# Kernel tuning notes

Hardware: AMD Instinct MI355X
Metric: run time of the kernel (lower is better)

The kernel has to match this reference:

```python
import jax, jax.numpy as jnp
import numpy as np

CLS_NUM = 2
SF = 8.0
STRIDE = 5
NO_OBJ_SCALE = 1.0
GAMMA = 1.0
B, C, H, W = 16, 8, 256, 256
NT = 256


def setup_inputs() -> dict:
    key = jax.random.key(0)
    k1, k2, k3, k4, k5, k6, k7 = jax.random.split(key, 7)
    predict = jax.random.normal(k1, (B, C, H, W), dtype=jnp.float32)
    b = jax.random.randint(k2, (NT,), 0, B).astype(jnp.float32)
    c = jax.random.randint(k3, (NT,), 0, CLS_NUM).astype(jnp.float32)
    cx = jax.random.uniform(k4, (NT,)) * (W * SF)   # image-scale coords
    cy = jax.random.uniform(k5, (NT,)) * (H * SF)
    wh = jax.random.uniform(k6, (NT, 2)) * 72.0 + 8.0  # box sizes in [8,80] px
    ang = (jax.random.uniform(k7, (NT,)) - 0.5) * np.pi
    targets = jnp.stack([b, c, cx, cy, wh[:, 0], wh[:, 1], ang], axis=1).astype(jnp.float32)
    return {"predict": predict, "targets": targets}


def _forward_loss(predict, targets):
    nB, nC, nH, nW = predict.shape
    N = targets.shape[0]
    pred = jnp.transpose(predict, (0, 2, 3, 1))  # [B,H,W,C]
    half = (STRIDE - 1) / 2.0
    x = jax.nn.sigmoid(pred[..., 0]) * STRIDE - half
    y = jax.nn.sigmoid(pred[..., 1]) * STRIDE - half
    w_p = pred[..., 2]
    h_p = pred[..., 3]
    p = jax.nn.sigmoid(pred[..., 4]) * 2.0 - 1.0
    q = jax.nn.sigmoid(pred[..., 5]) * 2.0 - 1.0

    # targets are detached in the torch code (numpy) -> no grad path
    tg = jax.lax.stop_gradient(targets)
    b_idx = tg[:, 0].astype(jnp.int32)
    cls_t = tg[:, 1].astype(jnp.int32)
    cx = tg[:, 2] / SF
    cy = tg[:, 3] / SF
    bw = tg[:, 4] / SF
    bh = tg[:, 5] / SF
    ang = tg[:, 6]
    ca, sa = jnp.cos(ang), jnp.sin(ang)

    # --- rotated-box rasterization for all boxes at once: [N,H,W] ---
    gx = jnp.arange(nW, dtype=jnp.float32) + 0.5
    gy = jnp.arange(nH, dtype=jnp.float32) + 0.5
    vx = gx[None, None, :] * ca[:, None, None] + gy[None, :, None] * sa[:, None, None]
    vy = -gx[None, None, :] * sa[:, None, None] + gy[None, :, None] * ca[:, None, None]
    bx = cx * ca + cy * sa
    by = -cx * sa + cy * ca
    x3 = (bx - bh / 2)[:, None, None]
    x4 = (bx + bh / 2)[:, None, None]
    y3 = (by - bw / 2)[:, None, None]
    y4 = (by + bw / 2)[:, None, None]
    inbox = (vx >= x3) & (vx <= x4) & (vy >= y3) & (vy <= y4)
    inexp = (vx >= x3 - 0.5) & (vx <= x4 + 0.5) & (vy >= y3 - 0.5) & (vy <= y4 + 0.5)

    # --- candidate grid cells around each box center (stride+1 window) ---
    lower = 0.5 - STRIDE / 2.0  # -2.0
    upper = 0.5 + STRIDE / 2.0  # 3.0
    K = STRIDE + 1
    i0 = jnp.floor(cx + lower).astype(jnp.int32)
    j0 = jnp.floor(cy + lower).astype(jnp.int32)
    I = jnp.broadcast_to((i0[:, None] + jnp.arange(K))[:, None, :], (N, K, K))
    J = jnp.broadcast_to((j0[:, None] + jnp.arange(K))[:, :, None], (N, K, K))
    ox = cx[:, None, None] - I.astype(jnp.float32)
    oy = cy[:, None, None] - J.astype(jnp.float32)
    inb = (I >= 0) & (I < nW) & (J >= 0) & (J < nH)
    off = (ox >= lower) & (ox <= upper) & (oy >= lower) & (oy <= upper)
    Ic = jnp.clip(I, 0, nW - 1)
    Jc = jnp.clip(J, 0, nH - 1)
    lin = ((b_idx[:, None, None] * nH + Jc) * nW + Ic).reshape(-1)
    SIZE = nB * nH * nW
    oxf = ox.reshape(-1)
    oyf = oy.reshape(-1)
    logw_f = jnp.broadcast_to(jnp.log(bw)[:, None, None], (N, K, K)).reshape(-1)
    logh_f = jnp.broadcast_to(jnp.log(bh)[:, None, None], (N, K, K)).reshape(-1)
    ang_f = jnp.broadcast_to(ang[:, None, None], (N, K, K)).reshape(-1)
    vflat = jnp.minimum(jnp.abs(oxf - 0.5), jnp.abs(oyf - 0.5))  # assignment priority

    total = jnp.float32(0.0)
    for c_id in range(CLS_NUM):
        cm = cls_t == c_id
        heat = jax.ops.segment_sum((inbox & cm[:, None, None]).astype(jnp.float32), b_idx, num_segments=nB) > 0
        cold = jax.ops.segment_sum((inexp & cm[:, None, None]).astype(jnp.float32), b_idx, num_segments=nB) == 0
        validf = (inb & off & cm[:, None, None]).reshape(-1)
        heat_at = heat.reshape(-1)[lin]
        cold_at = cold.reshape(-1)[lin]
        # noobj cleared at window cells overlapping the expanded rotated boxes
        clear_idx = jnp.where(validf & ~cold_at, lin, SIZE)
        noobj = jnp.ones(SIZE + 1, jnp.float32).at[clear_idx].set(0.0)[:SIZE]
        # per-cell min-priority box assignment (scatter-min + winner gather)
        elig = validf & heat_at
        vbig = jnp.where(elig, vflat, jnp.inf)
        minv = jnp.full(SIZE, jnp.inf, jnp.float32).at[lin].min(vbig)
        win = elig & (vbig <= minv[lin])
        widx = jnp.where(win, lin, SIZE)

        def scat(vals):
            return jnp.zeros(SIZE + 1, jnp.float32).at[widx].set(vals)[:SIZE]

        obj = jnp.zeros(SIZE + 1, jnp.float32).at[widx].set(1.0)[:SIZE]
        tx = scat(oxf).reshape(nB, nH, nW)
        ty = scat(oyf).reshape(nB, nH, nW)
        tw = scat(logw_f).reshape(nB, nH, nW)
        th = scat(logh_f).reshape(nB, nH, nW)
        ta = scat(ang_f).reshape(nB, nH, nW)
        obj = obj.reshape(nB, nH, nW)
        noobj = (noobj.reshape(nB, nH, nW)) * (1.0 - obj)

        n_obj = jnp.sum(obj)
        dn = jnp.maximum(n_obj, 1.0)
        n_no = jnp.sum(noobj)
        dno = jnp.maximum(n_no, 1.0)
        z = pred[..., 6 + c_id]  # conf logit; BCE(sigmoid(z), t) == softplus(+/-z)
        loss_conf_obj = jnp.sum(obj * jax.nn.softplus(-z)) / dn
        loss_conf_noobj = jnp.sum(noobj * jax.nn.softplus(z)) / dno

        def om(t):
            return jnp.sum(obj * t) / dn

        loss_x = om((x - tx) ** 2)
        loss_y = om((y - ty) ** 2)
        loss_w = om((w_p - tw) ** 2)
        loss_h = om((h_p - th) ** 2)
        wt = th - tw  # log(h)-log(w) at obj cells
        awt = jnp.abs(wt) ** GAMMA
        loss_angle = om(awt * (jnp.abs(p - jnp.cos(2.0 * ta)) + jnp.abs(q - jnp.sin(2.0 * ta))))
        loss_ring = om(jnp.abs(wt) * jnp.abs(p * p + q * q - 1.0))
        cls_loss = (loss_conf_obj + NO_OBJ_SCALE * loss_conf_noobj
                    + loss_x + loss_y + loss_w + loss_h + loss_angle + loss_ring)
        total = total + jnp.where(n_obj > 0, cls_loss, 0.0)
    return total


def reference(predict, targets):
    return _forward_loss(predict, targets)
```

## Files before the change

### kernel.cpp

```cpp
#include <hip/hip_runtime.h>
#include <math.h>

#define NTGT 256
#define NB 16
#define NH 256
#define NW 256
#define GSIZE (NB * NH * NW)

#define NENTBLK 36
#define NCONFBLK 256
#define PART 0
#define ENT  256

__device__ __forceinline__ float softplusf(float z) {
    return fmaxf(z, 0.0f) + log1pf(expf(-fabsf(z)));
}
__device__ __forceinline__ float sigmoidf(float t) {
    return 1.0f / (1.0f + expf(-t));
}

__global__ __launch_bounds__(256) void fused_main(const float* __restrict__ predict,
                                                  const float* __restrict__ targets,
                                                  float* __restrict__ ws) {
#pragma clang fp contract(off)
    const int t = threadIdx.x;

    if (blockIdx.x >= NENTBLK) {
        __shared__ float red[4];
        const int cb = blockIdx.x - NENTBLK;
        const int j = cb * 256 + t;
        const int ch  = 6 + ((j >> 14) & 1);
        const int pos = j & 16383;
        const int bhi = j >> 15;
        float s = 0.0f;
        for (int it = 0; it < 8; ++it) {
            const int b = it * 2 + bhi;
            const float4 v = *reinterpret_cast<const float4*>(
                predict + (size_t)(b * 8 + ch) * 65536 + (size_t)pos * 4);
            s += softplusf(v.x) + softplusf(v.y) + softplusf(v.z) + softplusf(v.w);
        }
        for (int o = 32; o > 0; o >>= 1) s += __shfl_down(s, o, 64);
        if ((t & 63) == 0) red[t >> 6] = s;
        __syncthreads();
        if (t == 0) ws[PART + cb] = red[0] + red[1] + red[2] + red[3];
        return;
    }

    __shared__ float s_raw[NTGT * 7];
    __shared__ float s_cx[NTGT], s_cy[NTGT], s_ca[NTGT], s_sa[NTGT];
    __shared__ float s_x3[NTGT], s_x4[NTGT], s_y3[NTGT], s_y4[NTGT];
    __shared__ int   s_i0[NTGT], s_j0[NTGT], s_g[NTGT], s_gl[NTGT];
    __shared__ int   s_gs[33];
    __shared__ int   cntg[32];
    __shared__ float blksum[16];
    __shared__ unsigned blkcnt[4];

    for (int i = t; i < NTGT * 7; i += 256) s_raw[i] = targets[i];
    if (t < 32) cntg[t] = 0;
    if (t < 16) blksum[t] = 0.0f;
    if (t >= 16 && t < 20) blkcnt[t - 16] = 0u;
    __syncthreads();

    {
        const float* T = &s_raw[t * 7];
        const int b   = (int)T[0];
        const int cls = (int)T[1];
        const float cx = T[2] * 0.125f, cy = T[3] * 0.125f;
        const float bw = T[4] * 0.125f, bh = T[5] * 0.125f;
        float sa, ca;
        sincosf(T[6], &sa, &ca);
        const float bx =  cx * ca + cy * sa;
        const float by = -cx * sa + cy * ca;
        const int g = b * 2 + cls;
        s_cx[t] = cx;  s_cy[t] = cy;
        s_ca[t] = ca;  s_sa[t] = sa;
        s_x3[t] = bx - bh * 0.5f;  s_x4[t] = bx + bh * 0.5f;
        s_y3[t] = by - bw * 0.5f;  s_y4[t] = by + bw * 0.5f;
        s_i0[t] = (int)floorf(cx - 2.0f);
        s_j0[t] = (int)floorf(cy - 2.0f);
        s_g[t]  = g;
        const int pos = atomicAdd(&cntg[g], 1);
        __syncthreads();
        if (t == 0) {
            int s = 0;
            for (int i = 0; i < 32; ++i) { s_gs[i] = s; s += cntg[i]; }
            s_gs[32] = s;
        }
        __syncthreads();
        s_gl[s_gs[g] + pos] = t;
    }
    __syncthreads();

    const int e = blockIdx.x * 256 + t;
    const int n = e / 36;
    const int sub = e - n * 36;
    const int kj = sub / 6;
    const int ki = sub - kj * 6;

    const int g = s_g[n];
    const int cls = g & 1;
    const int b = g >> 1;
    const int I = s_i0[n] + ki, J = s_j0[n] + kj;
    const float cx = s_cx[n], cy = s_cy[n];
    const float ox = cx - (float)I;
    const float oy = cy - (float)J;

    const bool validf = (I >= 0 && I < NW && J >= 0 && J < NH) &&
                        (ox >= -2.0f && ox <= 3.0f && oy >= -2.0f && oy <= 3.0f);

    bool isOwner = false, isWinC = false;
    const int gs = s_gs[g], ge = s_gs[g + 1];
    if (validf) {
        const float vfl = fminf(fabsf(ox - 0.5f), fabsf(oy - 0.5f));
        const unsigned long long mypack =
            ((unsigned long long)__float_as_uint(vfl) << 32) | (unsigned)e;
        unsigned long long best = mypack;
        int ownmin = e;
        for (int p = gs; p < ge; ++p) {
            const int m = s_gl[p];
            if (m == n) continue;
            const int kip = I - s_i0[m];
            if (kip < 0 || kip > 5) continue;
            const int kjp = J - s_j0[m];
            if (kjp < 0 || kjp > 5) continue;
            const float oxp = s_cx[m] - (float)I;
            const float oyp = s_cy[m] - (float)J;
            if (!(oxp >= -2.0f && oxp <= 3.0f && oyp >= -2.0f && oyp <= 3.0f)) continue;
            const int ep = (m * 6 + kjp) * 6 + kip;
            ownmin = min(ownmin, ep);
            const float vflp = fminf(fabsf(oxp - 0.5f), fabsf(oyp - 0.5f));
            const unsigned long long pk =
                ((unsigned long long)__float_as_uint(vflp) << 32) | (unsigned)ep;
            if (pk < best) best = pk;
        }
        isOwner = (ownmin == e);
        isWinC  = (best == mypack);
    }

    bool heat = false, anyexp = false;
    if (isOwner || isWinC) {
        const float gx = (float)I + 0.5f;
        const float gy = (float)J + 0.5f;
        for (int p = gs; p < ge; ++p) {
            const int m = s_gl[p];
            const float ca = s_ca[m], sa = s_sa[m];
            const float vx =  gx * ca + gy * sa;
            const float vy = -gx * sa + gy * ca;
            const float x3 = s_x3[m], x4 = s_x4[m];
            const float y3 = s_y3[m], y4 = s_y4[m];
            heat   |= (vx >= x3 && vx <= x4 && vy >= y3 && vy <= y4);
            anyexp |= (vx >= x3 - 0.5f && vx <= x4 + 0.5f &&
                       vy >= y3 - 0.5f && vy <= y4 + 0.5f);
        }
    }

    const size_t base = (size_t)b * 8 * 65536 + (size_t)J * 256 + (size_t)I;
    const bool doClear = isOwner && anyexp;
    const bool doWin   = isWinC && heat;

    float spz = 0.0f;
    if (doClear) spz = softplusf(predict[base + (size_t)(6 + cls) * 65536]);
    float v0 = (doClear && cls == 0) ? spz : 0.0f;
    float v1 = (doClear && cls == 1) ? spz : 0.0f;
    for (int o = 32; o > 0; o >>= 1) {
        v0 += __shfl_down(v0, o, 64);
        v1 += __shfl_down(v1, o, 64);
    }
    const unsigned long long m0 = __ballot(doClear && cls == 0);
    const unsigned long long m1 = __ballot(doClear && cls == 1);
    if ((t & 63) == 0) {
        if (v0 != 0.0f) atomicAdd(&blksum[14], v0);
        if (v1 != 0.0f) atomicAdd(&blksum[15], v1);
        if (m0) atomicAdd(&blkcnt[2], (unsigned)__popcll(m0));
        if (m1) atomicAdd(&blkcnt[3], (unsigned)__popcll(m1));
    }

    if (doWin) {
        const float p0 = predict[base];
        const float p1 = predict[base + 65536];
        const float p2 = predict[base + 2 * 65536];
        const float p3 = predict[base + 3 * 65536];
        const float p4 = predict[base + 4 * 65536];
        const float p5 = predict[base + 5 * 65536];
        const float z  = predict[base + (size_t)(6 + cls) * 65536];
        const float bw = s_raw[n * 7 + 4] * 0.125f;
        const float bh = s_raw[n * 7 + 5] * 0.125f;
        const float ang = s_raw[n * 7 + 6];
        const float xs = sigmoidf(p0) * 5.0f - 2.0f;
        const float ys = sigmoidf(p1) * 5.0f - 2.0f;
        const float pp = sigmoidf(p4) * 2.0f - 1.0f;
        const float qq = sigmoidf(p5) * 2.0f - 1.0f;
        const float tw = logf(bw), th = logf(bh);
        const float wt = th - tw, awt = fabsf(wt);
        float s2a, c2a;
        sincosf(2.0f * ang, &s2a, &c2a);
        atomicAdd(&blksum[0 + cls],  softplusf(-z));
        atomicAdd(&blksum[2 + cls],  (xs - ox) * (xs - ox));
        atomicAdd(&blksum[4 + cls],  (ys - oy) * (ys - oy));
        atomicAdd(&blksum[6 + cls],  (p2 - tw) * (p2 - tw));
        atomicAdd(&blksum[8 + cls],  (p3 - th) * (p3 - th));
        atomicAdd(&blksum[10 + cls], awt * (fabsf(pp - c2a) + fabsf(qq - s2a)));
        atomicAdd(&blksum[12 + cls], awt * fabsf(pp * pp + qq * qq - 1.0f));
        atomicAdd(&blkcnt[cls], 1u);
    }

    __syncthreads();
    if (t < 16) {
        ws[ENT + blockIdx.x * 20 + t] = blksum[t];
    } else if (t < 20) {
        ws[ENT + blockIdx.x * 20 + t] = (float)blkcnt[t - 16];
    }
}

__global__ __launch_bounds__(256) void final_kernel(const float* __restrict__ ws,
                                                    float* __restrict__ out) {
    __shared__ float r0[256], r1[256];
    __shared__ float esum[20];
    const int t = threadIdx.x;
    if (t < 20) esum[t] = 0.0f;
    const float v = ws[PART + t];
    const int c = (t >> 6) & 1;
    r0[t] = c ? 0.0f : v;
    r1[t] = c ? v : 0.0f;
    __syncthreads();
    for (int idx = t; idx < NENTBLK * 20; idx += 256) {
        const int slot = idx % 20;
        atomicAdd(&esum[slot], ws[ENT + idx]);
    }
    for (int o = 128; o > 0; o >>= 1) {
        __syncthreads();
        if (t < o) { r0[t] += r0[t + o]; r1[t] += r1[t + o]; }
    }
    __syncthreads();
    if (t == 0) {
        const float sAll[2] = { r0[0], r1[0] };
        float total = 0.0f;
        for (int c2 = 0; c2 < 2; ++c2) {
            const float nobj = esum[16 + c2];
            if (nobj > 0.0f) {
                const float dn  = nobj;
                const float dno = fmaxf((float)GSIZE - esum[18 + c2], 1.0f);
                total += esum[0 + c2] / dn
                       + (sAll[c2] - esum[14 + c2]) / dno
                       + (esum[2 + c2] + esum[4 + c2] + esum[6 + c2]
                          + esum[8 + c2] + esum[10 + c2] + esum[12 + c2]) / dn;
            }
        }
        out[0] = total;
    }
}

extern "C" void kernel_launch(void* const* d_in, const int* in_sizes, int n_in,
                              void* d_out, int out_size, void* d_ws, size_t ws_size,
                              hipStream_t stream) {
    const float* predict = (const float*)d_in[0];
    const float* targets = (const float*)d_in[1];
    float* out = (float*)d_out;
    float* ws = (float*)d_ws;

    fused_main<<<NENTBLK + NCONFBLK, 256, 0, stream>>>(predict, targets, ws);
    final_kernel<<<1, 256, 0, stream>>>(ws, out);
}
```

Measured before the change: 19.44 us.

## Merge final reduction into main kernel via cooperative grid sync

```diff
diff --git a/kernel.cpp b/kernel.cpp
--- a/kernel.cpp
+++ b/kernel.cpp
@@ -1,5 +1,8 @@
 #include <hip/hip_runtime.h>
+#include <hip/hip_cooperative_groups.h>
 #include <math.h>
+
+namespace cg = cooperative_groups;
 
 #define NTGT 256
 #define NB 16
@@ -9,6 +12,7 @@
 
 #define NENTBLK 36
 #define NCONFBLK 256
+#define NBLK (NENTBLK + NCONFBLK)
 #define PART 0
 #define ENT  256
 
@@ -19,15 +23,25 @@
     return 1.0f / (1.0f + expf(-t));
 }
 
-__global__ __launch_bounds__(256) void fused_main(const float* __restrict__ predict,
-                                                  const float* __restrict__ targets,
-                                                  float* __restrict__ ws) {
+__global__ __launch_bounds__(256) void fused_all(const float* __restrict__ predict,
+                                                 const float* __restrict__ targets,
+                                                 float* __restrict__ ws,
+                                                 float* __restrict__ out) {
 #pragma clang fp contract(off)
+    __shared__ float s_raw[NTGT * 7];
+    __shared__ float s_cx[NTGT], s_cy[NTGT], s_ca[NTGT], s_sa[NTGT];
+    __shared__ float s_x3[NTGT], s_x4[NTGT], s_y3[NTGT], s_y4[NTGT];
+    __shared__ int   s_i0[NTGT], s_j0[NTGT], s_g[NTGT], s_gl[NTGT];
+    __shared__ int   s_gs[33];
+    __shared__ int   cntg[32];
+    __shared__ float blksum[16];
+    __shared__ unsigned blkcnt[4];
+
     const int t = threadIdx.x;
-
-    if (blockIdx.x >= NENTBLK) {
-        __shared__ float red[4];
-        const int cb = blockIdx.x - NENTBLK;
+    const int bid = blockIdx.x;
+
+    if (bid >= NENTBLK) {
+        const int cb = bid - NENTBLK;
         const int j = cb * 256 + t;
         const int ch  = 6 + ((j >> 14) & 1);
         const int pos = j & 16383;
@@ -40,213 +54,205 @@
             s += softplusf(v.x) + softplusf(v.y) + softplusf(v.z) + softplusf(v.w);
         }
         for (int o = 32; o > 0; o >>= 1) s += __shfl_down(s, o, 64);
-        if ((t & 63) == 0) red[t >> 6] = s;
-        __syncthreads();
-        if (t == 0) ws[PART + cb] = red[0] + red[1] + red[2] + red[3];
-        return;
+        if ((t & 63) == 0) blksum[t >> 6] = s;
+        __syncthreads();
+        if (t == 0) ws[PART + cb] = blksum[0] + blksum[1] + blksum[2] + blksum[3];
+    } else {
+        for (int i = t; i < NTGT * 7; i += 256) s_raw[i] = targets[i];
+        if (t < 32) cntg[t] = 0;
+        if (t < 16) blksum[t] = 0.0f;
+        if (t >= 16 && t < 20) blkcnt[t - 16] = 0u;
+        __syncthreads();
+
+        {
+            const float* T = &s_raw[t * 7];
+            const int b   = (int)T[0];
+            const int cls = (int)T[1];
+            const float cx = T[2] * 0.125f, cy = T[3] * 0.125f;
+            const float bw = T[4] * 0.125f, bh = T[5] * 0.125f;
+            float sa, ca;
+            sincosf(T[6], &sa, &ca);
+            const float bx =  cx * ca + cy * sa;
+            const float by = -cx * sa + cy * ca;
+            const int g = b * 2 + cls;
+            s_cx[t] = cx;  s_cy[t] = cy;
+            s_ca[t] = ca;  s_sa[t] = sa;
+            s_x3[t] = bx - bh * 0.5f;  s_x4[t] = bx + bh * 0.5f;
+            s_y3[t] = by - bw * 0.5f;  s_y4[t] = by + bw * 0.5f;
+            s_i0[t] = (int)floorf(cx - 2.0f);
+            s_j0[t] = (int)floorf(cy - 2.0f);
+            s_g[t]  = g;
+            const int pos = atomicAdd(&cntg[g], 1);
+            __syncthreads();
+            if (t < 32) {
+                int sc = cntg[t];
+                for (int o = 1; o < 32; o <<= 1) {
+                    const int u = __shfl_up(sc, o, 64);
+                    if (t >= o) sc += u;
+                }
+                s_gs[t + 1] = sc;
+                if (t == 0) s_gs[0] = 0;
+            }
+            __syncthreads();
+            s_gl[s_gs[g] + pos] = t;
+        }
+        __syncthreads();
+
+        const int e = bid * 256 + t;
+        const int n = e / 36;
+        const int sub = e - n * 36;
+        const int kj = sub / 6;
+        const int ki = sub - kj * 6;
+
+        const int g = s_g[n];
+        const int cls = g & 1;
+        const int b = g >> 1;
+        const int I = s_i0[n] + ki, J = s_j0[n] + kj;
+        const float cx = s_cx[n], cy = s_cy[n];
+        const float ox = cx - (float)I;
+        const float oy = cy - (float)J;
+
+        const bool validf = (I >= 0 && I < NW && J >= 0 && J < NH) &&
+                            (ox >= -2.0f && ox <= 3.0f && oy >= -2.0f && oy <= 3.0f);
+
+        bool isOwner = false, isWinC = false;
+        const int gs = s_gs[g], ge = s_gs[g + 1];
+        if (validf) {
+            const float vfl = fminf(fabsf(ox - 0.5f), fabsf(oy - 0.5f));
+            const unsigned long long mypack =
+                ((unsigned long long)__float_as_uint(vfl) << 32) | (unsigned)e;
+            unsigned long long best = mypack;
+            int ownmin = e;
+            for (int p = gs; p < ge; ++p) {
+                const int m = s_gl[p];
+                if (m == n) continue;
+                const int kip = I - s_i0[m];
+                if (kip < 0 || kip > 5) continue;
+                const int kjp = J - s_j0[m];
+                if (kjp < 0 || kjp > 5) continue;
+                const float oxp = s_cx[m] - (float)I;
+                const float oyp = s_cy[m] - (float)J;
+                if (!(oxp >= -2.0f && oxp <= 3.0f && oyp >= -2.0f && oyp <= 3.0f)) continue;
+                const int ep = (m * 6 + kjp) * 6 + kip;
+                ownmin = min(ownmin, ep);
+                const float vflp = fminf(fabsf(oxp - 0.5f), fabsf(oyp - 0.5f));
+                const unsigned long long pk =
+                    ((unsigned long long)__float_as_uint(vflp) << 32) | (unsigned)ep;
+                if (pk < best) best = pk;
+            }
+            isOwner = (ownmin == e);
+            isWinC  = (best == mypack);
+        }
+
+        bool heat = false, anyexp = false;
+        if (isOwner || isWinC) {
+            const float gx = (float)I + 0.5f;
+            const float gy = (float)J + 0.5f;
+            for (int p = gs; p < ge; ++p) {
+                const int m = s_gl[p];
+                const float ca = s_ca[m], sa = s_sa[m];
+                const float vx =  gx * ca + gy * sa;
+                const float vy = -gx * sa + gy * ca;
+                const float x3 = s_x3[m], x4 = s_x4[m];
+                const float y3 = s_y3[m], y4 = s_y4[m];
+                heat   |= (vx >= x3 && vx <= x4 && vy >= y3 && vy <= y4);
+                anyexp |= (vx >= x3 - 0.5f && vx <= x4 + 0.5f &&
+                           vy >= y3 - 0.5f && vy <= y4 + 0.5f);
+            }
+        }
+
+        const size_t base = (size_t)b * 8 * 65536 + (size_t)J * 256 + (size_t)I;
+        const bool doClear = isOwner && anyexp;
+        const bool doWin   = isWinC && heat;
+
+        float spz = 0.0f;
+        if (doClear) spz = softplusf(predict[base + (size_t)(6 + cls) * 65536]);
+        float v0 = (doClear && cls == 0) ? spz : 0.0f;
+        float v1 = (doClear && cls == 1) ? spz : 0.0f;
+        for (int o = 32; o > 0; o >>= 1) {
+            v0 += __shfl_down(v0, o, 64);
+            v1 += __shfl_down(v1, o, 64);
+        }
+        const unsigned long long m0 = __ballot(doClear && cls == 0);
+        const unsigned long long m1 = __ballot(doClear && cls == 1);
+        if ((t & 63) == 0) {
+            if (v0 != 0.0f) atomicAdd(&blksum[14], v0);
+            if (v1 != 0.0f) atomicAdd(&blksum[15], v1);
+            if (m0) atomicAdd(&blkcnt[2], (unsigned)__popcll(m0));
+            if (m1) atomicAdd(&blkcnt[3], (unsigned)__popcll(m1));
+        }
+
+        if (doWin) {
+            const float p0 = predict[base];
+            const float p1 = predict[base + 65536];
+            const float p2 = predict[base + 2 * 65536];
+            const float p3 = predict[base + 3 * 65536];
+            const float p4 = predict[base + 4 * 65536];
+            const float p5 = predict[base + 5 * 65536];
+            const float z  = predict[base + (size_t)(6 + cls) * 65536];
+            const float bw = s_raw[n * 7 + 4] * 0.125f;
+            const float bh = s_raw[n * 7 + 5] * 0.125f;
+            const float ang = s_raw[n * 7 + 6];
+            const float xs = sigmoidf(p0) * 5.0f - 2.0f;
+            const float ys = sigmoidf(p1) * 5.0f - 2.0f;
+            const float pp = sigmoidf(p4) * 2.0f - 1.0f;
+            const float qq = sigmoidf(p5) * 2.0f - 1.0f;
+            const float tw = logf(bw), th = logf(bh);
+            const float wt = th - tw, awt = fabsf(wt);
+            float s2a, c2a;
+            sincosf(2.0f * ang, &s2a, &c2a);
+            atomicAdd(&blksum[0 + cls],  softplusf(-z));
+            atomicAdd(&blksum[2 + cls],  (xs - ox) * (xs - ox));
+            atomicAdd(&blksum[4 + cls],  (ys - oy) * (ys - oy));
+            atomicAdd(&blksum[6 + cls],  (p2 - tw) * (p2 - tw));
+            atomicAdd(&blksum[8 + cls],  (p3 - th) * (p3 - th));
+            atomicAdd(&blksum[10 + cls], awt * (fabsf(pp - c2a) + fabsf(qq - s2a)));
+            atomicAdd(&blksum[12 + cls], awt * fabsf(pp * pp + qq * qq - 1.0f));
+            atomicAdd(&blkcnt[cls], 1u);
+        }
+
+        __syncthreads();
+        if (t < 16) {
+            ws[ENT + bid * 20 + t] = blksum[t];
+        } else if (t < 20) {
+            ws[ENT + bid * 20 + t] = (float)blkcnt[t - 16];
+        }
     }
 
-    __shared__ float s_raw[NTGT * 7];
-    __shared__ float s_cx[NTGT], s_cy[NTGT], s_ca[NTGT], s_sa[NTGT];
-    __shared__ float s_x3[NTGT], s_x4[NTGT], s_y3[NTGT], s_y4[NTGT];
-    __shared__ int   s_i0[NTGT], s_j0[NTGT], s_g[NTGT], s_gl[NTGT];
-    __shared__ int   s_gs[33];
-    __shared__ int   cntg[32];
-    __shared__ float blksum[16];
-    __shared__ unsigned blkcnt[4];
-
-    for (int i = t; i < NTGT * 7; i += 256) s_raw[i] = targets[i];
-    if (t < 32) cntg[t] = 0;
-    if (t < 16) blksum[t] = 0.0f;
-    if (t >= 16 && t < 20) blkcnt[t - 16] = 0u;
-    __syncthreads();
-
-    {
-        const float* T = &s_raw[t * 7];
-        const int b   = (int)T[0];
-        const int cls = (int)T[1];
-        const float cx = T[2] * 0.125f, cy = T[3] * 0.125f;
-        const float bw = T[4] * 0.125f, bh = T[5] * 0.125f;
-        float sa, ca;
-        sincosf(T[6], &sa, &ca);
-        const float bx =  cx * ca + cy * sa;
-        const float by = -cx * sa + cy * ca;
-        const int g = b * 2 + cls;
-        s_cx[t] = cx;  s_cy[t] = cy;
-        s_ca[t] = ca;  s_sa[t] = sa;
-        s_x3[t] = bx - bh * 0.5f;  s_x4[t] = bx + bh * 0.5f;
-        s_y3[t] = by - bw * 0.5f;  s_y4[t] = by + bw * 0.5f;
-        s_i0[t] = (int)floorf(cx - 2.0f);
-        s_j0[t] = (int)floorf(cy - 2.0f);
-        s_g[t]  = g;
-        const int pos = atomicAdd(&cntg[g], 1);
+    __threadfence();
+    cg::this_grid().sync();
+
+    if (bid == 0) {
+        if (t < 20) s_sa[t] = 0.0f;
+        const float v = ws[PART + t];
+        const int c = (t >> 6) & 1;
+        s_cx[t] = c ? 0.0f : v;
+        s_cy[t] = c ? v : 0.0f;
+        __syncthreads();
+        for (int idx = t; idx < NENTBLK * 20; idx += 256) {
+            atomicAdd(&s_sa[idx % 20], ws[ENT + idx]);
+        }
+        for (int o = 128; o > 0; o >>= 1) {
+            __syncthreads();
+            if (t < o) { s_cx[t] += s_cx[t + o]; s_cy[t] += s_cy[t + o]; }
+        }
         __syncthreads();
         if (t == 0) {
-            int s = 0;
-            for (int i = 0; i < 32; ++i) { s_gs[i] = s; s += cntg[i]; }
-            s_gs[32] = s;
-        }
-        __syncthreads();
-        s_gl[s_gs[g] + pos] = t;
-    }
-    __syncthreads();
-
-    const int e = blockIdx.x * 256 + t;
-    const int n = e / 36;
-    const int sub = e - n * 36;
-    const int kj = sub / 6;
-    const int ki = sub - kj * 6;
-
-    const int g = s_g[n];
-    const int cls = g & 1;
-    const int b = g >> 1;
-    const int I = s_i0[n] + ki, J = s_j0[n] + kj;
-    const float cx = s_cx[n], cy = s_cy[n];
-    const float ox = cx - (float)I;
-    const float oy = cy - (float)J;
-
-    const bool validf = (I >= 0 && I < NW && J >= 0 && J < NH) &&
-                        (ox >= -2.0f && ox <= 3.0f && oy >= -2.0f && oy <= 3.0f);
-
-    bool isOwner = false, isWinC = false;
-    const int gs = s_gs[g], ge = s_gs[g + 1];
-    if (validf) {
-        const float vfl = fminf(fabsf(ox - 0.5f), fabsf(oy - 0.5f));
-        const unsigned long long mypack =
-            ((unsigned long long)__float_as_uint(vfl) << 32) | (unsigned)e;
-        unsigned long long best = mypack;
-        int ownmin = e;
-        for (int p = gs; p < ge; ++p) {
-            const int m = s_gl[p];
-            if (m == n) continue;
-            const int kip = I - s_i0[m];
-            if (kip < 0 || kip > 5) continue;
-            const int kjp = J - s_j0[m];
-            if (kjp < 0 || kjp > 5) continue;
-            const float oxp = s_cx[m] - (float)I;
-            const float oyp = s_cy[m] - (float)J;
-            if (!(oxp >= -2.0f && oxp <= 3.0f && oyp >= -2.0f && oyp <= 3.0f)) continue;
-            const int ep = (m * 6 + kjp) * 6 + kip;
-            ownmin = min(ownmin, ep);
-            const float vflp = fminf(fabsf(oxp - 0.5f), fabsf(oyp - 0.5f));
-            const unsigned long long pk =
-                ((unsigned long long)__float_as_uint(vflp) << 32) | (unsigned)ep;
-            if (pk < best) best = pk;
-        }
-        isOwner = (ownmin == e);
-        isWinC  = (best == mypack);
-    }
-
-    bool heat = false, anyexp = false;
-    if (isOwner || isWinC) {
-        const float gx = (float)I + 0.5f;
-        const float gy = (float)J + 0.5f;
-        for (int p = gs; p < ge; ++p) {
-            const int m = s_gl[p];
-            const float ca = s_ca[m], sa = s_sa[m];
-            const float vx =  gx * ca + gy * sa;
-            const float vy = -gx * sa + gy * ca;
-            const float x3 = s_x3[m], x4 = s_x4[m];
-            const float y3 = s_y3[m], y4 = s_y4[m];
-            heat   |= (vx >= x3 && vx <= x4 && vy >= y3 && vy <= y4);
-            anyexp |= (vx >= x3 - 0.5f && vx <= x4 + 0.5f &&
-                       vy >= y3 - 0.5f && vy <= y4 + 0.5f);
-        }
-    }
-
-    const size_t base = (size_t)b * 8 * 65536 + (size_t)J * 256 + (size_t)I;
-    const bool doClear = isOwner && anyexp;
-    const bool doWin   = isWinC && heat;
-
-    float spz = 0.0f;
-    if (doClear) spz = softplusf(predict[base + (size_t)(6 + cls) * 65536]);
-    float v0 = (doClear && cls == 0) ? spz : 0.0f;
-    float v1 = (doClear && cls == 1) ? spz : 0.0f;
-    for (int o = 32; o > 0; o >>= 1) {
-        v0 += __shfl_down(v0, o, 64);
-        v1 += __shfl_down(v1, o, 64);
-    }
-    const unsigned long long m0 = __ballot(doClear && cls == 0);
-    const unsigned long long m1 = __ballot(doClear && cls == 1);
-    if ((t & 63) == 0) {
-        if (v0 != 0.0f) atomicAdd(&blksum[14], v0);
-        if (v1 != 0.0f) atomicAdd(&blksum[15], v1);
-        if (m0) atomicAdd(&blkcnt[2], (unsigned)__popcll(m0));
-        if (m1) atomicAdd(&blkcnt[3], (unsigned)__popcll(m1));
-    }
-
-    if (doWin) {
-        const float p0 = predict[base];
-        const float p1 = predict[base + 65536];
-        const float p2 = predict[base + 2 * 65536];
-        const float p3 = predict[base + 3 * 65536];
-        const float p4 = predict[base + 4 * 65536];
-        const float p5 = predict[base + 5 * 65536];
-        const float z  = predict[base + (size_t)(6 + cls) * 65536];
-        const float bw = s_raw[n * 7 + 4] * 0.125f;
-        const float bh = s_raw[n * 7 + 5] * 0.125f;
-        const float ang = s_raw[n * 7 + 6];
-        const float xs = sigmoidf(p0) * 5.0f - 2.0f;
-        const float ys = sigmoidf(p1) * 5.0f - 2.0f;
-        const float pp = sigmoidf(p4) * 2.0f - 1.0f;
-        const float qq = sigmoidf(p5) * 2.0f - 1.0f;
-        const float tw = logf(bw), th = logf(bh);
-        const float wt = th - tw, awt = fabsf(wt);
-        float s2a, c2a;
-        sincosf(2.0f * ang, &s2a, &c2a);
-        atomicAdd(&blksum[0 + cls],  softplusf(-z));
-        atomicAdd(&blksum[2 + cls],  (xs - ox) * (xs - ox));
-        atomicAdd(&blksum[4 + cls],  (ys - oy) * (ys - oy));
-        atomicAdd(&blksum[6 + cls],  (p2 - tw) * (p2 - tw));
-        atomicAdd(&blksum[8 + cls],  (p3 - th) * (p3 - th));
-        atomicAdd(&blksum[10 + cls], awt * (fabsf(pp - c2a) + fabsf(qq - s2a)));
-        atomicAdd(&blksum[12 + cls], awt * fabsf(pp * pp + qq * qq - 1.0f));
-        atomicAdd(&blkcnt[cls], 1u);
-    }
-
-    __syncthreads();
-    if (t < 16) {
-        ws[ENT + blockIdx.x * 20 + t] = blksum[t];
-    } else if (t < 20) {
-        ws[ENT + blockIdx.x * 20 + t] = (float)blkcnt[t - 16];
-    }
-}
-
-__global__ __launch_bounds__(256) void final_kernel(const float* __restrict__ ws,
-                                                    float* __restrict__ out) {
-    __shared__ float r0[256], r1[256];
-    __shared__ float esum[20];
-    const int t = threadIdx.x;
-    if (t < 20) esum[t] = 0.0f;
-    const float v = ws[PART + t];
-    const int c = (t >> 6) & 1;
-    r0[t] = c ? 0.0f : v;
-    r1[t] = c ? v : 0.0f;
-    __syncthreads();
-    for (int idx = t; idx < NENTBLK * 20; idx += 256) {
-        const int slot = idx % 20;
-        atomicAdd(&esum[slot], ws[ENT + idx]);
-    }
-    for (int o = 128; o > 0; o >>= 1) {
-        __syncthreads();
-        if (t < o) { r0[t] += r0[t + o]; r1[t] += r1[t + o]; }
-    }
-    __syncthreads();
-    if (t == 0) {
-        const float sAll[2] = { r0[0], r1[0] };
-        float total = 0.0f;
-        for (int c2 = 0; c2 < 2; ++c2) {
-            const float nobj = esum[16 + c2];
-            if (nobj > 0.0f) {
-                const float dn  = nobj;
-                const float dno = fmaxf((float)GSIZE - esum[18 + c2], 1.0f);
-                total += esum[0 + c2] / dn
-                       + (sAll[c2] - esum[14 + c2]) / dno
-                       + (esum[2 + c2] + esum[4 + c2] + esum[6 + c2]
-                          + esum[8 + c2] + esum[10 + c2] + esum[12 + c2]) / dn;
-            }
-        }
-        out[0] = total;
+            const float sAll[2] = { s_cx[0], s_cy[0] };
+            float total = 0.0f;
+            for (int c2 = 0; c2 < 2; ++c2) {
+                const float nobj = s_sa[16 + c2];
+                if (nobj > 0.0f) {
+                    const float dn  = nobj;
+                    const float dno = fmaxf((float)GSIZE - s_sa[18 + c2], 1.0f);
+                    total += s_sa[0 + c2] / dn
+                           + (sAll[c2] - s_sa[14 + c2]) / dno
+                           + (s_sa[2 + c2] + s_sa[4 + c2] + s_sa[6 + c2]
+                              + s_sa[8 + c2] + s_sa[10 + c2] + s_sa[12 + c2]) / dn;
+                }
+            }
+            out[0] = total;
+        }
     }
 }
 
@@ -258,6 +264,7 @@
     float* out = (float*)d_out;
     float* ws = (float*)d_ws;
 
-    fused_main<<<NENTBLK + NCONFBLK, 256, 0, stream>>>(predict, targets, ws);
-    final_kernel<<<1, 256, 0, stream>>>(ws, out);
-}
+    void* args[] = { (void*)&predict, (void*)&targets, (void*)&ws, (void*)&out };
+    hipLaunchCooperativeKernel((const void*)fused_all, dim3(NBLK), dim3(256),
+                               args, 0, stream);
+}
```

After: 71.23 us. 266% more time.
